# Kernel tuning notes

Hardware: AMD Instinct MI355X
Metric: run time of the kernel (lower is better)

## Reference

```python
import jax, jax.numpy as jnp
import numpy as np

# dims
B, N, L = 8, 128, 512          # batch, n_vars, context_window
PL, ST = 16, 8                  # patch_len, stride
PN = (L - PL) // ST + 1         # patch_num = 63
DM, H, DFF, NL = 128, 16, 256, 2
DK = DM // H
DG, MP, BETA = 8, 3, 0.05       # d_gcn, mp_layers, propbeta
TW = 96                         # target_window


def setup_inputs() -> dict:
    key = jax.random.key(0)
    ks = iter(jax.random.split(key, 64))
    def nrm(shape, s=0.02):
        return jax.random.normal(next(ks), shape, jnp.float32) * s
    inp = {
        "x": jax.random.normal(next(ks), (B, N, L), jnp.float32),
        "adj_logits": jax.random.normal(next(ks), (B, L, N, N), jnp.float32),
        # DGCN params
        "dgcn_start_w": nrm((1, DG)), "dgcn_start_b": jnp.zeros((DG,), jnp.float32),
        "dgcn_mlp_w": nrm(((MP + 1) * DG, 1)), "dgcn_mlp_b": jnp.zeros((1,), jnp.float32),
        # patch embedding + positional
        "W_P": nrm((PL, DM)), "b_P": jnp.zeros((DM,), jnp.float32), "W_pos": nrm((PN, DM)),
        # encoder layers (stacked over NL)
        "Wq": nrm((NL, DM, DM)), "bq": jnp.zeros((NL, DM), jnp.float32),
        "Wk": nrm((NL, DM, DM)), "bk": jnp.zeros((NL, DM), jnp.float32),
        "Wv": nrm((NL, DM, DM)), "bv": jnp.zeros((NL, DM), jnp.float32),
        "Wo": nrm((NL, DM, DM)), "bo": jnp.zeros((NL, DM), jnp.float32),
        "scale": jnp.full((NL,), DK ** -0.5, jnp.float32),
        "bn1_g": jnp.ones((NL, DM), jnp.float32), "bn1_b": jnp.zeros((NL, DM), jnp.float32),
        "ff_w1": nrm((NL, DM, DFF)), "ff_b1": jnp.zeros((NL, DFF), jnp.float32),
        "ff_w2": nrm((NL, DFF, DM)), "ff_b2": jnp.zeros((NL, DM), jnp.float32),
        "bn2_g": jnp.ones((NL, DM), jnp.float32), "bn2_b": jnp.zeros((NL, DM), jnp.float32),
        # head
        "head_w": nrm((DM * PN, TW)), "head_b": jnp.zeros((TW,), jnp.float32),
    }
    return inp


def _bn(x, g, b):
    # BatchNorm1d in training mode over (batch, seq) per feature channel
    mu = x.mean(axis=(0, 1))
    var = x.var(axis=(0, 1))
    return (x - mu) * jax.lax.rsqrt(var + 1e-5) * g + b


def reference(x, adj_logits, dgcn_start_w, dgcn_start_b, dgcn_mlp_w, dgcn_mlp_b,
              W_P, b_P, W_pos, Wq, bq, Wk, bk, Wv, bv, Wo, bo, scale,
              bn1_g, bn1_b, ff_w1, ff_b1, ff_w2, ff_b2, bn2_g, bn2_b,
              head_w, head_b):
    # ---- DGCN: multi-hop diffusion over variables, per time step ----
    x4 = x[..., None]                                   # [b,n,s,1]
    A = jax.nn.softmax(adj_logits, axis=2)              # [b,s,n,m], normalized over source n
    a = jnp.transpose(A, (0, 2, 3, 1))                  # [b,n,m,s]
    h = x4 @ dgcn_start_w + dgcn_start_b                # [b,n,s,d_gcn]
    outs = [h]
    for _ in range(MP):
        h = BETA * x4 + (1.0 - BETA) * jnp.einsum('bnsc,bnms->bmsc', h, a)
        outs.append(h)
    y = (jnp.concatenate(outs, axis=-1) @ dgcn_mlp_w + dgcn_mlp_b)[..., 0]  # [b,n,s]
    # ---- patching ----
    win = jnp.arange(PN)[:, None] * ST + jnp.arange(PL)[None, :]
    z = y[:, :, win]                                    # [b,n,pn,pl]
    # ---- TSTiEncoder (channel independent) ----
    src = (z @ W_P + b_P).reshape(B * N, PN, DM) + W_pos
    prev = None
    for l in range(NL):
        q = (src @ Wq[l] + bq[l]).reshape(-1, PN, H, DK).transpose(0, 2, 1, 3)
        k = (src @ Wk[l] + bk[l]).reshape(-1, PN, H, DK).transpose(0, 2, 1, 3)
        v = (src @ Wv[l] + bv[l]).reshape(-1, PN, H, DK).transpose(0, 2, 1, 3)
        scores = jnp.einsum('bhqd,bhkd->bhqk', q, k) * scale[l]
        if prev is not None:
            scores = scores + prev                      # residual attention
        w = jax.nn.softmax(scores, axis=-1)
        o = jnp.einsum('bhqk,bhkd->bhqd', w, v).transpose(0, 2, 1, 3).reshape(-1, PN, DM)
        src = _bn(src + (o @ Wo[l] + bo[l]), bn1_g[l], bn1_b[l])
        ff = jax.nn.gelu(src @ ff_w1[l] + ff_b1[l], approximate=False) @ ff_w2[l] + ff_b2[l]
        src = _bn(src + ff, bn2_g[l], bn2_b[l])
        prev = scores
    # ---- Flatten_Head ----
    enc = src.reshape(B, N, PN, DM).transpose(0, 1, 3, 2).reshape(B, N, DM * PN)
    return enc @ head_w + head_b                        # [b, n_vars, target_window]
```

## Files before the change

kernel.cpp:

```cpp
#include <hip/hip_runtime.h>
#include <hip/hip_bf16.h>
#include <math.h>

#define RM 64512

typedef short short8 __attribute__((ext_vector_type(8)));
typedef float f32x4 __attribute__((ext_vector_type(4)));
typedef unsigned short ushort4v __attribute__((ext_vector_type(4)));
typedef unsigned short ushort8v __attribute__((ext_vector_type(8)));

__device__ __forceinline__ float gelu_f(float v) {
    return 0.5f * v * (1.0f + erff(v * 0.70710678118654752f));
}
__device__ __forceinline__ float b2f(unsigned short u) {
    unsigned int x = ((unsigned int)u) << 16;
    return __builtin_bit_cast(float, x);
}
__device__ __forceinline__ unsigned short f2b(float f) {
    __hip_bfloat16 h = __float2bfloat16(f);
    return __builtin_bit_cast(unsigned short, h);
}

__global__ __launch_bounds__(256) void dgcn_kernel(
    const float* __restrict__ x, const float* __restrict__ adj,
    const float* __restrict__ sw, const float* __restrict__ sb,
    const float* __restrict__ mw, const float* __restrict__ mb,
    float* __restrict__ y,
    const float* __restrict__ Wq, const float* __restrict__ Wk, const float* __restrict__ Wv,
    const float* __restrict__ Wo, const float* __restrict__ fw1, const float* __restrict__ fw2,
    const float* __restrict__ bq, const float* __restrict__ bk, const float* __restrict__ bv,
    unsigned short* __restrict__ WB, float* __restrict__ bcat)
{
    if (blockIdx.x >= 4096) {
        const int wb = blockIdx.x - 4096;
        const int id = wb / 64, bx = wb % 64;
        const int l = id / 6, mat = id % 6;
        const float* src; int K, N; size_t off = (size_t)l * 131072;
        switch (mat) {
            case 0: src = Wq  + l*16384; K = 128; N = 128; off += 0;      break;
            case 1: src = Wk  + l*16384; K = 128; N = 128; off += 16384;  break;
            case 2: src = Wv  + l*16384; K = 128; N = 128; off += 32768;  break;
            case 3: src = Wo  + l*16384; K = 128; N = 128; off += 49152;  break;
            case 4: src = fw1 + l*32768; K = 128; N = 256; off += 65536;  break;
            default:src = fw2 + l*32768; K = 256; N = 128; off += 98304;  break;
        }
        const int total = K * N;
        const int ksh = (K == 256) ? 8 : 7;
        for (int idx = bx*256 + threadIdx.x; idx < total; idx += 64*256) {
            int n = idx >> ksh, k = idx & (K - 1);
            WB[off + idx] = f2b(src[(size_t)k*N + n]);
        }
        if (id == 0 && bx == 0) {
            for (int idx = threadIdx.x; idx < 768; idx += 256) {
                int ll = idx / 384, j = idx % 384;
                float vv;
                if (j < 128)      vv = bq[ll*128 + j];
                else if (j < 256) vv = bk[ll*128 + j - 128];
                else              vv = bv[ll*128 + j - 256];
                bcat[idx] = vv;
            }
        }
        return;
    }
    __shared__ __align__(16) unsigned short ET[128*128];
    __shared__ __align__(16) unsigned short hT[16*128];
    __shared__ float red[256];
    __shared__ float iv[128];
    __shared__ float xc[128];
    __shared__ float yac[128];
    const int bid = blockIdx.x;
    const int b = bid >> 9, s = bid & 511;
    const int t = threadIdx.x;
    const int lane = t & 63, wid = t >> 6;
    const float* ap = adj + (size_t)bid * 16384;

    if (t < 128) xc[t] = x[((size_t)b*128 + t)*512 + s];

    {
        const int m = t & 127, ng = t >> 7;
        float sm = 0.f;
        for (int p = 0; p < 16; ++p) {
            const int n0 = p*8 + ng*4;
            float e0 = __expf(ap[(size_t)(n0+0)*128 + m]);
            float e1 = __expf(ap[(size_t)(n0+1)*128 + m]);
            float e2 = __expf(ap[(size_t)(n0+2)*128 + m]);
            float e3 = __expf(ap[(size_t)(n0+3)*128 + m]);
            sm += e0 + e1 + e2 + e3;
            ushort4v u4; u4[0]=f2b(e0); u4[1]=f2b(e1); u4[2]=f2b(e2); u4[3]=f2b(e3);
            *(ushort4v*)((char*)ET + m*256 + (((n0>>3) ^ (m & 15))*16) + (n0 & 7)*2) = u4;
        }
        red[ng*128 + m] = sm;
        *(ushort4v*)&hT[8*128 + t*4] = (ushort4v){0,0,0,0};
    }
    __syncthreads();
    if (t < 128) iv[t] = 1.f / (red[t] + red[128 + t]);
    if (t < 128) {
        const int m = t;
        const float xm = xc[m];
        float yp = 0.f;
        #pragma unroll
        for (int c = 0; c < 8; ++c) {
            float h = xm*sw[c] + sb[c];
            yp += h*mw[c];
            *(unsigned short*)((char*)hT + c*256 + ((((m>>3) ^ c))*16) + (m & 7)*2) = f2b(h);
        }
        yac[m] = yp;
    }
    __syncthreads();

    const int rl = lane & 15, kh = lane >> 4;
    short8 af[2][4];
    float xr[2][4], ivr[2][4];
    #pragma unroll
    for (int ti = 0; ti < 2; ++ti) {
        const int mrow = (wid*2 + ti)*16 + rl;
        #pragma unroll
        for (int ks = 0; ks < 4; ++ks) {
            const int ch = (ks*4 + kh) ^ (mrow & 15);
            af[ti][ks] = *(const short8*)((const char*)ET + mrow*256 + ch*16);
        }
        #pragma unroll
        for (int r = 0; r < 4; ++r) {
            const int m = (wid*2 + ti)*16 + kh*4 + r;
            xr[ti][r]  = 0.05f * xc[m];
            ivr[ti][r] = 0.95f * iv[m];
        }
    }
    float yl[2][4] = {};
    #pragma unroll
    for (int step = 1; step <= 3; ++step) {
        short8 bfr[4];
        #pragma unroll
        for (int ks = 0; ks < 4; ++ks) {
            const int ch = (ks*4 + kh) ^ rl;
            bfr[ks] = *(const short8*)((const char*)hT + rl*256 + ch*16);
        }
        f32x4 acc[2] = {};
        #pragma unroll
        for (int ti = 0; ti < 2; ++ti)
            #pragma unroll
            for (int ks = 0; ks < 4; ++ks)
                acc[ti] = __builtin_amdgcn_mfma_f32_16x16x32_bf16(af[ti][ks], bfr[ks], acc[ti], 0, 0, 0);
        __syncthreads();
        const float mwc = (rl < 8) ? mw[step*8 + rl] : 0.f;
        #pragma unroll
        for (int ti = 0; ti < 2; ++ti) {
            const int m0 = (wid*2 + ti)*16 + kh*4;
            ushort4v hw4;
            float hnew[4];
            #pragma unroll
            for (int r = 0; r < 4; ++r) {
                float v = xr[ti][r] + ivr[ti][r]*acc[ti][r];
                hnew[r] = v;
                hw4[r] = f2b(v);
            }
            *(ushort4v*)((char*)hT + rl*256 + (((m0>>3) ^ rl)*16) + (m0 & 7)*2) = hw4;
            #pragma unroll
            for (int r = 0; r < 4; ++r) {
                float vv = hnew[r]*mwc;
                vv += __shfl_xor(vv, 1);
                vv += __shfl_xor(vv, 2);
                vv += __shfl_xor(vv, 4);
                vv += __shfl_xor(vv, 8);
                yl[ti][r] += vv;
            }
        }
        __syncthreads();
    }
    if (rl == 0) {
        #pragma unroll
        for (int ti = 0; ti < 2; ++ti)
            #pragma unroll
            for (int r = 0; r < 4; ++r)
                yac[(wid*2 + ti)*16 + kh*4 + r] += yl[ti][r];
    }
    __syncthreads();
    if (t < 128) y[((size_t)b*128 + t)*512 + s] = yac[t] + mb[0];
}

__global__ __launch_bounds__(256) void patch_kernel(
    const float* __restrict__ y, const float* __restrict__ Wp, const float* __restrict__ bp,
    const float* __restrict__ Wpos, unsigned short* __restrict__ srcb)
{
    __shared__ float ys[512];
    __shared__ float wps[16*128];
    const int bn = blockIdx.x;
    const int t = threadIdx.x;
    ys[t]       = y[(size_t)bn*512 + t];
    ys[t + 256] = y[(size_t)bn*512 + t + 256];
    #pragma unroll
    for (int r = 0; r < 8; ++r) wps[t + r*256] = Wp[t + r*256];
    __syncthreads();
    for (int cu = t; cu < 1008; cu += 256) {
        int p = cu >> 4, d0 = (cu & 15) * 8;
        float o[8];
        #pragma unroll
        for (int j = 0; j < 8; ++j) o[j] = bp[d0+j] + Wpos[p*128 + d0 + j];
        #pragma unroll
        for (int tt = 0; tt < 16; ++tt) {
            float a = ys[p*8 + tt];
            #pragma unroll
            for (int j = 0; j < 8; ++j) o[j] += a * wps[tt*128 + d0 + j];
        }
        size_t row = (size_t)bn*63 + p;
        ushort8v u;
        #pragma unroll
        for (int j = 0; j < 8; ++j) u[j] = f2b(o[j]);
        *(ushort8v*)&srcb[row*128 + d0] = u;
    }
}

template<int ACT, int OM, int RESMODE, bool STATS, bool AHM, int NB, int KK>
__global__ __launch_bounds__(256) void mgemm(
    const unsigned short* __restrict__ A, const unsigned short* __restrict__ WB,
    const float* __restrict__ bias, const unsigned short* __restrict__ Rsd,
    const float* __restrict__ snR,
    unsigned short* __restrict__ Cb,
    float* __restrict__ part)
{
    constexpr int NTOT = NB * 128;
    constexpr int kch = KK >> 3;
    constexpr int KT = KK >> 7;
    __shared__ __align__(16) unsigned short AsL[64*128];
    __shared__ __align__(16) unsigned short BsL[128*128];
    __shared__ float sred[4][16][8], qred[4][16][8];
    const int t = threadIdx.x;
    const int lane = t & 63, wid = t >> 6;
    const int wr = wid >> 1, wc = wid & 1;
    const int m0 = blockIdx.x * 64;
    const int kh = lane >> 4, rl = lane & 15;
    const int rq = lane >> 4;
    float sj[8] = {}, qj[8] = {};

    for (int ib = 0; ib < NB; ++ib) {
        f32x4 acc[2][4] = {};
        for (int kt = 0; kt < KT; ++kt) {
            if (ib == 0 || KT > 1) {
                #pragma unroll
                for (int i = 0; i < 4; ++i) {
                    int cid = i*256 + t;
                    const unsigned short* ga;
                    if constexpr (AHM) {
                        int hd2 = cid >> 6, row = cid & 63;
                        ga = A + ((size_t)hd2*RM + (m0+row))*8;
                    } else {
                        int row = cid >> 4, c = cid & 15;
                        int c_g = c ^ (row & 7);
                        ga = A + ((size_t)(m0+row)*kch + kt*16 + c_g)*8;
                    }
                    __builtin_amdgcn_global_load_lds((const unsigned int*)ga,
                        (unsigned int*)&AsL[(i*256 + wid*64)*8], 16, 0, 0);
                }
            }
            #pragma unroll
            for (int i = 0; i < 8; ++i) {
                int cid = i*256 + t;
                int nr = cid >> 4, c = cid & 15;
                const unsigned short* gb = WB + (size_t)ib*128*KK
                    + ((size_t)nr*kch + kt*16 + (c ^ (nr & 7)))*8;
                __builtin_amdgcn_global_load_lds((const unsigned int*)gb,
                    (unsigned int*)&BsL[(i*256 + wid*64)*8], 16, 0, 0);
            }
            __syncthreads();
            #pragma unroll
            for (int ks = 0; ks < 4; ++ks) {
                const int cA = ks*4 + kh;
                short8 af[2], bfr[4];
                #pragma unroll
                for (int i = 0; i < 2; ++i) {
                    int row = wr*32 + i*16 + rl;
                    if constexpr (AHM) af[i] = *(const short8*)&AsL[(cA*64 + row)*8];
                    else               af[i] = *(const short8*)&AsL[row*128 + ((cA ^ (row & 7))*8)];
                }
                #pragma unroll
                for (int j = 0; j < 4; ++j) {
                    int cn = wc*64 + j*16 + rl;
                    bfr[j] = *(const short8*)&BsL[cn*128 + ((cA ^ (cn & 7))*8)];
                }
                #pragma unroll
                for (int i = 0; i < 2; ++i)
                    #pragma unroll
                    for (int j = 0; j < 4; ++j)
                        acc[i][j] = __builtin_amdgcn_mfma_f32_16x16x32_bf16(af[i], bfr[j], acc[i][j], 0, 0, 0);
            }
            __syncthreads();
        }
        #pragma unroll
        for (int j = 0; j < 4; ++j) {
            const int col_l = wc*64 + j*16 + rl;
            const float bs = bias[ib*128 + col_l];
            const int chunk = col_l >> 3, bo2 = (col_l & 7) << 1;
            #pragma unroll
            for (int i = 0; i < 2; ++i) {
                #pragma unroll
                for (int r = 0; r < 4; ++r) {
                    const int row_l = wr*32 + i*16 + rq*4 + r;
                    float v = acc[i][j][r] + bs;
                    if constexpr (ACT == 1) v = gelu_f(v);
                    *(unsigned short*)((char*)BsL + row_l*256 + ((chunk ^ (row_l & 15))<<4) + bo2) = f2b(v);
                }
            }
        }
        __syncthreads();
        if constexpr (OM == 1) {
            #pragma unroll
            for (int it = 0; it < 4; ++it) {
                int cid = it*256 + t;
                int row_l = cid & 63, hd_l = cid >> 6;
                ushort8v u = *(const ushort8v*)((const char*)BsL + row_l*256 + ((hd_l ^ (row_l & 15))<<4));
                *(ushort8v*)&Cb[(((size_t)(ib*16 + hd_l))*RM + m0 + row_l)*8] = u;
            }
        } else {
            #pragma unroll
            for (int it = 0; it < 4; ++it) {
                const int row_l = it*16 + (t >> 4), c = t & 15;
                ushort8v u = *(const ushort8v*)((const char*)BsL + row_l*256 + ((c ^ (row_l & 15))<<4));
                const size_t gbase = (size_t)(m0 + row_l)*NTOT + ib*128 + c*8;
                ushort8v rs = {};
                if constexpr (RESMODE != 0) rs = *(const ushort8v*)&Rsd[gbase];
                ushort8v o8;
                #pragma unroll
                for (int jj = 0; jj < 8; ++jj) {
                    float v = b2f(u[jj]);
                    if constexpr (RESMODE == 1) v += b2f(rs[jj]);
                    if constexpr (RESMODE == 2) v += b2f(rs[jj])*snR[c*8+jj] + snR[128 + c*8 + jj];
                    if constexpr (STATS) { sj[jj] += v; qj[jj] += v*v; }
                    o8[jj] = f2b(v);
                }
                *(ushort8v*)&Cb[gbase] = o8;
            }
        }
        __syncthreads();
    }
    if constexpr (STATS) {
        #pragma unroll
        for (int jj = 0; jj < 8; ++jj) {
            sj[jj] += __shfl_xor(sj[jj], 16); qj[jj] += __shfl_xor(qj[jj], 16);
            sj[jj] += __shfl_xor(sj[jj], 32); qj[jj] += __shfl_xor(qj[jj], 32);
        }
        if ((lane >> 4) == 0) {
            #pragma unroll
            for (int jj = 0; jj < 8; ++jj) {
                sred[wid][lane][jj] = sj[jj];
                qred[wid][lane][jj] = qj[jj];
            }
        }
        __syncthreads();
        if (t < 128) {
            const int c2 = t >> 3, jj = t & 7;
            float s = sred[0][c2][jj] + sred[1][c2][jj] + sred[2][c2][jj] + sred[3][c2][jj];
            float q = qred[0][c2][jj] + qred[1][c2][jj] + qred[2][c2][jj] + qred[3][c2][jj];
            part[(size_t)blockIdx.x*256 + t]       = s;
            part[(size_t)blockIdx.x*256 + 128 + t] = q;
        }
    }
}

__global__ __launch_bounds__(256) void bnred(const float* __restrict__ part,
    const float* __restrict__ g, const float* __restrict__ b, float* __restrict__ sn)
{
    const int c = blockIdx.x, t = threadIdx.x;
    float s = 0.f, q = 0.f;
    for (int bid = t; bid < 1008; bid += 256) {
        s += part[(size_t)bid*256 + c];
        q += part[(size_t)bid*256 + 128 + c];
    }
    __shared__ float ls[256], lq[256];
    ls[t] = s; lq[t] = q;
    __syncthreads();
    for (int o = 128; o > 0; o >>= 1) {
        if (t < o) { ls[t] += ls[t+o]; lq[t] += lq[t+o]; }
        __syncthreads();
    }
    if (t == 0) {
        const float invM = 1.f / (float)RM;
        float mean = ls[0] * invM;
        float var  = fmaxf(lq[0]*invM - mean*mean, 0.f);
        float sc = g[c] * rsqrtf(var + 1e-5f);
        sn[c]       = sc;
        sn[128 + c] = b[c] - mean*sc;
    }
}

__global__ __launch_bounds__(256) void wfold(const unsigned short* __restrict__ WBs,
    const float* __restrict__ sn, const float* __restrict__ bsrc,
    unsigned short* __restrict__ WBd, float* __restrict__ bdst)
{
    const int t = threadIdx.x, wv = t >> 6, lane = t & 63;
    const int n = blockIdx.x*4 + wv;
    float w1 = b2f(WBs[(size_t)n*128 + lane]);
    float w2 = b2f(WBs[(size_t)n*128 + 64 + lane]);
    WBd[(size_t)n*128 + lane]      = f2b(sn[lane]*w1);
    WBd[(size_t)n*128 + 64 + lane] = f2b(sn[64+lane]*w2);
    float bacc = sn[128+lane]*w1 + sn[192+lane]*w2;
    #pragma unroll
    for (int msk = 1; msk < 64; msk <<= 1) bacc += __shfl_xor(bacc, msk);
    if (lane == 0) bdst[n] = bsrc[n] + bacc;
}

template<int L>
__global__ __launch_bounds__(256) void attn_kernel(
    const unsigned short* __restrict__ qkv, const unsigned short* __restrict__ qkvP,
    const float* __restrict__ scale, unsigned short* __restrict__ ob)
{
    __shared__ float ks[4][504], vs[4][504], k0s[4][504];
    const int bn = blockIdx.x;
    const int t = threadIdx.x, wid = t >> 6, lane = t & 63;
    const int hd = blockIdx.y*4 + wid;
    const size_t rbase = (size_t)hd*RM + (size_t)bn*63;
    float qr[8] = {}, q0r[8] = {};
    if (lane < 63) {
        ushort8v ku = *(const ushort8v*)&qkv[((size_t)16*RM*8) + (rbase + lane)*8];
        ushort8v vu = *(const ushort8v*)&qkv[((size_t)32*RM*8) + (rbase + lane)*8];
        #pragma unroll
        for (int d = 0; d < 8; ++d) { ks[wid][lane*8+d] = b2f(ku[d]); vs[wid][lane*8+d] = b2f(vu[d]); }
        ushort8v qu = *(const ushort8v*)&qkv[(rbase + lane)*8];
        #pragma unroll
        for (int d = 0; d < 8; ++d) qr[d] = b2f(qu[d]);
        if constexpr (L > 0) {
            ushort8v k0u = *(const ushort8v*)&qkvP[((size_t)16*RM*8) + (rbase + lane)*8];
            #pragma unroll
            for (int d = 0; d < 8; ++d) k0s[wid][lane*8+d] = b2f(k0u[d]);
            ushort8v q0u = *(const ushort8v*)&qkvP[(rbase + lane)*8];
            #pragma unroll
            for (int d = 0; d < 8; ++d) q0r[d] = b2f(q0u[d]);
        }
    }
    __syncthreads();
    if (lane >= 63) return;
    const float scl  = scale[L];
    const float scl0 = (L > 0) ? scale[0] : 0.f;
    float sum = 0.f;
    float oa[8] = {};
    for (int j = 0; j < 63; ++j) {
        float s = 0.f;
        #pragma unroll
        for (int d = 0; d < 8; ++d) s += qr[d]*ks[wid][j*8+d];
        s *= scl;
        if constexpr (L > 0) {
            float s0 = 0.f;
            #pragma unroll
            for (int d = 0; d < 8; ++d) s0 += q0r[d]*k0s[wid][j*8+d];
            s += scl0 * s0;
        }
        float p = __expf(s);
        sum += p;
        #pragma unroll
        for (int d = 0; d < 8; ++d) oa[d] += p*vs[wid][j*8+d];
    }
    float inv = 1.f / sum;
    ushort8v u;
    #pragma unroll
    for (int d = 0; d < 8; ++d) u[d] = f2b(oa[d]*inv);
    *(ushort8v*)&ob[((size_t)hd*RM + (size_t)bn*63 + lane)*8] = u;
}

__global__ __launch_bounds__(256) void hprep(
    const float* __restrict__ hw, const float* __restrict__ hb,
    const float* __restrict__ sn,
    unsigned short* __restrict__ hwTf, float* __restrict__ hbf)
{
    const int t = threadIdx.x;
    if (blockIdx.x < 63) {
        const int p = blockIdx.x;
        for (int idx = t; idx < 16384; idx += 256) {
            int n = idx >> 7, d = idx & 127;
            unsigned short w = 0;
            if (n < 96) w = f2b(sn[d] * hw[(size_t)(d*63 + p)*96 + n]);
            hwTf[((size_t)p*128 + n)*128 + d] = w;
        }
    } else {
        const int n = blockIdx.x - 63;
        float acc = 0.f;
        for (int k = t; k < 8064; k += 256) {
            int d = (int)(((unsigned)k * 33289u) >> 21);
            acc += sn[128 + d] * hw[(size_t)k*96 + n];
        }
        __shared__ float ls[256];
        ls[t] = acc;
        __syncthreads();
        for (int o = 128; o > 0; o >>= 1) { if (t < o) ls[t] += ls[t+o]; __syncthreads(); }
        if (t == 0) hbf[n] = hb[n] + ls[0];
    }
}

__global__ __launch_bounds__(256) void mhead(
    const unsigned short* __restrict__ A, const unsigned short* __restrict__ BW,
    float* __restrict__ part)
{
    __shared__ __align__(16) unsigned short AsL[128*128];
    __shared__ __align__(16) unsigned short BsL[128*128];
    const int t = threadIdx.x;
    const int lane = t & 63, wid = t >> 6;
    const int wr = wid >> 1, wc = wid & 1;
    const int m0 = blockIdx.x * 128;
    const int p  = blockIdx.y;
    #pragma unroll
    for (int i = 0; i < 8; ++i) {
        int cid = i*256 + t;
        int row = cid >> 4, c = cid & 15;
        const unsigned short* ga = A + ((size_t)(m0+row)*63 + p)*128 + ((c ^ (row & 7))*8);
        __builtin_amdgcn_global_load_lds((const unsigned int*)ga,
            (unsigned int*)&AsL[(i*256 + wid*64)*8], 16, 0, 0);
    }
    #pragma unroll
    for (int i = 0; i < 8; ++i) {
        int cid = i*256 + t;
        int nr = cid >> 4, c = cid & 15;
        const unsigned short* gb = BW + ((size_t)p*128 + nr)*128 + ((c ^ (nr & 7))*8);
        __builtin_amdgcn_global_load_lds((const unsigned int*)gb,
            (unsigned int*)&BsL[(i*256 + wid*64)*8], 16, 0, 0);
    }
    __syncthreads();
    const int kh = lane >> 4, rl = lane & 15;
    f32x4 acc[4][3] = {};
    #pragma unroll
    for (int kq = 0; kq < 4; ++kq) {
        const int cA = kq*4 + kh;
        short8 af[4], bfr[3];
        #pragma unroll
        for (int i = 0; i < 4; ++i) {
            int row = wr*64 + i*16 + rl;
            af[i] = *(const short8*)&AsL[row*128 + ((cA ^ (row & 7))*8)];
        }
        #pragma unroll
        for (int j = 0; j < 3; ++j) {
            int cn = wc*48 + j*16 + rl;
            bfr[j] = *(const short8*)&BsL[cn*128 + ((cA ^ (cn & 7))*8)];
        }
        #pragma unroll
        for (int i = 0; i < 4; ++i)
            #pragma unroll
            for (int j = 0; j < 3; ++j)
                acc[i][j] = __builtin_amdgcn_mfma_f32_16x16x32_bf16(af[i], bfr[j], acc[i][j], 0, 0, 0);
    }
    const int rl2 = lane & 15, rq = lane >> 4;
    #pragma unroll
    for (int j = 0; j < 3; ++j) {
        const int col = wc*48 + j*16 + rl2;
        #pragma unroll
        for (int i = 0; i < 4; ++i) {
            const int rbase = m0 + wr*64 + i*16 + rq*4;
            #pragma unroll
            for (int r = 0; r < 4; ++r)
                part[((size_t)p*1024 + rbase + r)*96 + col] = acc[i][j][r];
        }
    }
}

__global__ __launch_bounds__(256) void head_reduce(const float* __restrict__ part,
    const float* __restrict__ hbf, float* __restrict__ out)
{
    int idx = blockIdx.x*256 + threadIdx.x;
    float s = hbf[idx % 96];
    #pragma unroll
    for (int blk = 0; blk < 63; ++blk) s += part[(size_t)blk*98304 + idx];
    out[idx] = s;
}

extern "C" void kernel_launch(void* const* d_in, const int* in_sizes, int n_in,
                              void* d_out, int out_size, void* d_ws, size_t ws_size,
                              hipStream_t stream) {
    const float* x    = (const float*)d_in[0];
    const float* adj  = (const float*)d_in[1];
    const float* sw   = (const float*)d_in[2];
    const float* sb   = (const float*)d_in[3];
    const float* mw   = (const float*)d_in[4];
    const float* mb   = (const float*)d_in[5];
    const float* Wp   = (const float*)d_in[6];
    const float* bp   = (const float*)d_in[7];
    const float* Wpos = (const float*)d_in[8];
    const float* Wq   = (const float*)d_in[9];
    const float* bq   = (const float*)d_in[10];
    const float* Wk   = (const float*)d_in[11];
    const float* bk   = (const float*)d_in[12];
    const float* Wv   = (const float*)d_in[13];
    const float* bv   = (const float*)d_in[14];
    const float* Wo   = (const float*)d_in[15];
    const float* bo   = (const float*)d_in[16];
    const float* scale= (const float*)d_in[17];
    const float* bn1g = (const float*)d_in[18];
    const float* bn1b = (const float*)d_in[19];
    const float* fw1  = (const float*)d_in[20];
    const float* fb1  = (const float*)d_in[21];
    const float* fw2  = (const float*)d_in[22];
    const float* fb2  = (const float*)d_in[23];
    const float* bn2g = (const float*)d_in[24];
    const float* bn2b = (const float*)d_in[25];
    const float* hw   = (const float*)d_in[26];
    const float* hb   = (const float*)d_in[27];
    float* out = (float*)d_out;

    float* y     = (float*)d_ws;
    float* part  = y     + 524288;
    float* snorm = part  + 258048;
    float* bcat  = snorm + 1024;
    float* bfold = bcat  + 768;
    float* hbf   = bfold + 1024;
    float* hpart = hbf   + 128;
    unsigned short* srcb = (unsigned short*)(hpart + 6193152);
    unsigned short* t1b  = srcb + 8257536;
    unsigned short* t2b  = t1b  + 8257536;
    unsigned short* g    = t2b  + 8257536;
    unsigned short* o_bf = g    + 16515072;
    unsigned short* qkv0 = o_bf + 8257536;
    unsigned short* qkv1 = qkv0 + 24772608;
    unsigned short* WB   = qkv1 + 24772608;
    unsigned short* WF   = WB   + 262144;
    unsigned short* hwTf = WF   + 131072;

    dgcn_kernel<<<4864, 256, 0, stream>>>(x, adj, sw, sb, mw, mb, y,
        Wq, Wk, Wv, Wo, fw1, fw2, bq, bk, bv, WB, bcat);
    patch_kernel<<<1024, 256, 0, stream>>>(y, Wp, bp, Wpos, srcb);

    mgemm<0,1,0,false,false,3,128><<<1008, 256, 0, stream>>>(srcb, WB, bcat, nullptr, nullptr, qkv0, nullptr);
    attn_kernel<0><<<dim3(1024,4), 256, 0, stream>>>(qkv0, qkv0, scale, o_bf);
    mgemm<0,2,1,true,true,1,128><<<1008, 256, 0, stream>>>(o_bf, WB + 49152, bo, srcb, nullptr, t1b, part);
    bnred<<<128, 256, 0, stream>>>(part, bn1g, bn1b, snorm);
    wfold<<<64, 256, 0, stream>>>(WB + 65536, snorm, fb1, WF, bfold);
    mgemm<1,2,0,false,false,2,128><<<1008, 256, 0, stream>>>(t1b, WF, bfold, nullptr, nullptr, g, nullptr);
    mgemm<0,2,2,true,false,1,256><<<1008, 256, 0, stream>>>(g, WB + 98304, fb2, t1b, snorm, t2b, part);
    bnred<<<128, 256, 0, stream>>>(part, bn2g, bn2b, snorm + 256);
    wfold<<<96, 256, 0, stream>>>(WB + 131072, snorm + 256, bcat + 384, WF + 65536, bfold + 512);

    mgemm<0,1,0,false,false,3,128><<<1008, 256, 0, stream>>>(t2b, WF + 65536, bfold + 512, nullptr, nullptr, qkv1, nullptr);
    attn_kernel<1><<<dim3(1024,4), 256, 0, stream>>>(qkv1, qkv0, scale, o_bf);
    mgemm<0,2,2,true,true,1,128><<<1008, 256, 0, stream>>>(o_bf, WB + 131072 + 49152, bo + 128, t2b, snorm + 256, t1b, part);
    bnred<<<128, 256, 0, stream>>>(part, bn1g + 128, bn1b + 128, snorm + 512);
    wfold<<<64, 256, 0, stream>>>(WB + 131072 + 65536, snorm + 512, fb1 + 256, WF + 32768, bfold + 256);
    mgemm<1,2,0,false,false,2,128><<<1008, 256, 0, stream>>>(t1b, WF + 32768, bfold + 256, nullptr, nullptr, g, nullptr);
    mgemm<0,2,2,true,false,1,256><<<1008, 256, 0, stream>>>(g, WB + 131072 + 98304, fb2 + 128, t1b, snorm + 512, t2b, part);
    bnred<<<128, 256, 0, stream>>>(part, bn2g + 128, bn2b + 128, snorm + 768);

    hprep<<<159, 256, 0, stream>>>(hw, hb, snorm + 768, hwTf, hbf);
    mhead<<<dim3(8,63), 256, 0, stream>>>(t2b, hwTf, hpart);
    head_reduce<<<384, 256, 0, stream>>>(hpart, hbf, out);
}
```

Measured before the change: 393.2 us.

## Fuse FFN up-projection, GELU and down-projection into one kernel

Replaces the two feed-forward GEMM launches per layer with a single kernel. It computes the 256-wide GELU hidden tile for 64 rows, keeps it in shared memory, and multiplies it by W2 in place. The residual add and the BatchNorm partial-sum epilogue are kept in the same kernel. This removes the global write and re-read of the large hidden activation tensor g and one launch per layer. The cost is 80KB of shared memory per block, which lowers occupancy, and W1 and W2 loads are serialised rather than pipelined.

```diff
diff --git a/kernel.cpp b/kernel.cpp
--- a/kernel.cpp
+++ b/kernel.cpp
@@ -353,6 +353,183 @@
             part[(size_t)blockIdx.x*256 + t]       = s;
             part[(size_t)blockIdx.x*256 + 128 + t] = q;
         }
+    }
+}
+
+__global__ __launch_bounds__(256) void ffused(
+    const unsigned short* __restrict__ A, const unsigned short* __restrict__ W1,
+    const float* __restrict__ b1, const unsigned short* __restrict__ W2,
+    const float* __restrict__ b2, const unsigned short* __restrict__ Rsd,
+    const float* __restrict__ snR,
+    unsigned short* __restrict__ Cb, float* __restrict__ part)
+{
+    __shared__ __align__(16) char smem[81920];
+    unsigned short* AsL = (unsigned short*)smem;
+    unsigned short* BsL = (unsigned short*)(smem + 16384);
+    unsigned short* G   = (unsigned short*)(smem + 49152);
+    float* sred = (float*)(smem + 49152);
+    float* qred = sred + 512;
+    const int t = threadIdx.x;
+    const int lane = t & 63, wid = t >> 6;
+    const int wr = wid >> 1, wc = wid & 1;
+    const int m0 = blockIdx.x * 64;
+    const int kh = lane >> 4, rl = lane & 15;
+    const int rq = lane >> 4;
+
+    #pragma unroll
+    for (int i = 0; i < 4; ++i) {
+        int cid = i*256 + t;
+        int row = cid >> 4, c = cid & 15;
+        const unsigned short* ga = A + ((size_t)(m0+row)*16 + (c ^ (row & 7)))*8;
+        __builtin_amdgcn_global_load_lds((const unsigned int*)ga,
+            (unsigned int*)&AsL[(i*256 + wid*64)*8], 16, 0, 0);
+    }
+    #pragma unroll
+    for (int i = 0; i < 8; ++i) {
+        int cid = i*256 + t;
+        int nr = cid >> 4, c = cid & 15;
+        const unsigned short* gb = W1 + ((size_t)nr*16 + (c ^ (nr & 7)))*8;
+        __builtin_amdgcn_global_load_lds((const unsigned int*)gb,
+            (unsigned int*)&BsL[(i*256 + wid*64)*8], 16, 0, 0);
+    }
+    __syncthreads();
+    for (int ib = 0; ib < 2; ++ib) {
+        f32x4 acc[2][4] = {};
+        #pragma unroll
+        for (int ks = 0; ks < 4; ++ks) {
+            const int cA = ks*4 + kh;
+            short8 af[2], bfr[4];
+            #pragma unroll
+            for (int i = 0; i < 2; ++i) {
+                int row = wr*32 + i*16 + rl;
+                af[i] = *(const short8*)&AsL[row*128 + ((cA ^ (row & 7))*8)];
+            }
+            #pragma unroll
+            for (int j = 0; j < 4; ++j) {
+                int cn = wc*64 + j*16 + rl;
+                bfr[j] = *(const short8*)&BsL[cn*128 + ((cA ^ (cn & 7))*8)];
+            }
+            #pragma unroll
+            for (int i = 0; i < 2; ++i)
+                #pragma unroll
+                for (int j = 0; j < 4; ++j)
+                    acc[i][j] = __builtin_amdgcn_mfma_f32_16x16x32_bf16(af[i], bfr[j], acc[i][j], 0, 0, 0);
+        }
+        __syncthreads();
+        if (ib == 0) {
+            #pragma unroll
+            for (int i = 0; i < 8; ++i) {
+                int cid = i*256 + t;
+                int nr = cid >> 4, c = cid & 15;
+                const unsigned short* gb = W1 + ((size_t)(128+nr)*16 + (c ^ (nr & 7)))*8;
+                __builtin_amdgcn_global_load_lds((const unsigned int*)gb,
+                    (unsigned int*)&BsL[(i*256 + wid*64)*8], 16, 0, 0);
+            }
+        }
+        #pragma unroll
+        for (int j = 0; j < 4; ++j) {
+            const int col_l = wc*64 + j*16 + rl;
+            const int colg = ib*128 + col_l;
+            const float bs = b1[colg];
+            const int cg = colg >> 3, bo2 = (colg & 7) << 1;
+            #pragma unroll
+            for (int i = 0; i < 2; ++i) {
+                #pragma unroll
+                for (int r = 0; r < 4; ++r) {
+                    const int row_l = wr*32 + i*16 + rq*4 + r;
+                    float v = gelu_f(acc[i][j][r] + bs);
+                    *(unsigned short*)((char*)G + row_l*512 + (((cg ^ (row_l & 15)))<<4) + bo2) = f2b(v);
+                }
+            }
+        }
+        __syncthreads();
+    }
+    f32x4 acc2[2][4] = {};
+    for (int kt = 0; kt < 2; ++kt) {
+        #pragma unroll
+        for (int i = 0; i < 8; ++i) {
+            int cid = i*256 + t;
+            int nr = cid >> 4, c = cid & 15;
+            const unsigned short* gb = W2 + ((size_t)nr*32 + kt*16 + (c ^ (nr & 7)))*8;
+            __builtin_amdgcn_global_load_lds((const unsigned int*)gb,
+                (unsigned int*)&BsL[(i*256 + wid*64)*8], 16, 0, 0);
+        }
+        __syncthreads();
+        #pragma unroll
+        for (int ks = 0; ks < 4; ++ks) {
+            const int cA = ks*4 + kh;
+            short8 af[2], bfr[4];
+            #pragma unroll
+            for (int i = 0; i < 2; ++i) {
+                int row = wr*32 + i*16 + rl;
+                af[i] = *(const short8*)((const char*)G + row*512 + ((((kt*16 + cA) ^ (row & 15)))<<4));
+            }
+            #pragma unroll
+            for (int j = 0; j < 4; ++j) {
+                int cn = wc*64 + j*16 + rl;
+                bfr[j] = *(const short8*)&BsL[cn*128 + ((cA ^ (cn & 7))*8)];
+            }
+            #pragma unroll
+            for (int i = 0; i < 2; ++i)
+                #pragma unroll
+                for (int j = 0; j < 4; ++j)
+                    acc2[i][j] = __builtin_amdgcn_mfma_f32_16x16x32_bf16(af[i], bfr[j], acc2[i][j], 0, 0, 0);
+        }
+        __syncthreads();
+    }
+    #pragma unroll
+    for (int j = 0; j < 4; ++j) {
+        const int col_l = wc*64 + j*16 + rl;
+        const float bs = b2[col_l];
+        const int chunk = col_l >> 3, bo2 = (col_l & 7) << 1;
+        #pragma unroll
+        for (int i = 0; i < 2; ++i) {
+            #pragma unroll
+            for (int r = 0; r < 4; ++r) {
+                const int row_l = wr*32 + i*16 + rq*4 + r;
+                *(unsigned short*)((char*)AsL + row_l*256 + ((chunk ^ (row_l & 15))<<4) + bo2)
+                    = f2b(acc2[i][j][r] + bs);
+            }
+        }
+    }
+    __syncthreads();
+    float sj[8] = {}, qj[8] = {};
+    #pragma unroll
+    for (int it = 0; it < 4; ++it) {
+        const int row_l = it*16 + (t >> 4), c = t & 15;
+        ushort8v u = *(const ushort8v*)((const char*)AsL + row_l*256 + ((c ^ (row_l & 15))<<4));
+        const size_t gbase = (size_t)(m0 + row_l)*128 + c*8;
+        ushort8v rs = *(const ushort8v*)&Rsd[gbase];
+        ushort8v o8;
+        #pragma unroll
+        for (int jj = 0; jj < 8; ++jj) {
+            float v = b2f(u[jj]) + b2f(rs[jj])*snR[c*8+jj] + snR[128 + c*8 + jj];
+            sj[jj] += v; qj[jj] += v*v;
+            o8[jj] = f2b(v);
+        }
+        *(ushort8v*)&Cb[gbase] = o8;
+    }
+    #pragma unroll
+    for (int jj = 0; jj < 8; ++jj) {
+        sj[jj] += __shfl_xor(sj[jj], 16); qj[jj] += __shfl_xor(qj[jj], 16);
+        sj[jj] += __shfl_xor(sj[jj], 32); qj[jj] += __shfl_xor(qj[jj], 32);
+    }
+    if ((lane >> 4) == 0) {
+        #pragma unroll
+        for (int jj = 0; jj < 8; ++jj) {
+            sred[wid*128 + lane*8 + jj] = sj[jj];
+            qred[wid*128 + lane*8 + jj] = qj[jj];
+        }
+    }
+    __syncthreads();
+    if (t < 128) {
+        const int c2 = t >> 3, jj = t & 7;
+        float s = sred[0*128 + c2*8 + jj] + sred[1*128 + c2*8 + jj]
+                + sred[2*128 + c2*8 + jj] + sred[3*128 + c2*8 + jj];
+        float q = qred[0*128 + c2*8 + jj] + qred[1*128 + c2*8 + jj]
+                + qred[2*128 + c2*8 + jj] + qred[3*128 + c2*8 + jj];
+        part[(size_t)blockIdx.x*256 + t]       = s;
+        part[(size_t)blockIdx.x*256 + 128 + t] = q;
     }
 }
 
@@ -618,8 +795,7 @@
     mgemm<0,2,1,true,true,1,128><<<1008, 256, 0, stream>>>(o_bf, WB + 49152, bo, srcb, nullptr, t1b, part);
     bnred<<<128, 256, 0, stream>>>(part, bn1g, bn1b, snorm);
     wfold<<<64, 256, 0, stream>>>(WB + 65536, snorm, fb1, WF, bfold);
-    mgemm<1,2,0,false,false,2,128><<<1008, 256, 0, stream>>>(t1b, WF, bfold, nullptr, nullptr, g, nullptr);
-    mgemm<0,2,2,true,false,1,256><<<1008, 256, 0, stream>>>(g, WB + 98304, fb2, t1b, snorm, t2b, part);
+    ffused<<<1008, 256, 0, stream>>>(t1b, WF, bfold, WB + 98304, fb2, t1b, snorm, t2b, part);
     bnred<<<128, 256, 0, stream>>>(part, bn2g, bn2b, snorm + 256);
     wfold<<<96, 256, 0, stream>>>(WB + 131072, snorm + 256, bcat + 384, WF + 65536, bfold + 512);
 
@@ -628,8 +804,7 @@
     mgemm<0,2,2,true,true,1,128><<<1008, 256, 0, stream>>>(o_bf, WB + 131072 + 49152, bo + 128, t2b, snorm + 256, t1b, part);
     bnred<<<128, 256, 0, stream>>>(part, bn1g + 128, bn1b + 128, snorm + 512);
     wfold<<<64, 256, 0, stream>>>(WB + 131072 + 65536, snorm + 512, fb1 + 256, WF + 32768, bfold + 256);
-    mgemm<1,2,0,false,false,2,128><<<1008, 256, 0, stream>>>(t1b, WF + 32768, bfold + 256, nullptr, nullptr, g, nullptr);
-    mgemm<0,2,2,true,false,1,256><<<1008, 256, 0, stream>>>(g, WB + 131072 + 98304, fb2 + 128, t1b, snorm + 512, t2b, part);
+    ffused<<<1008, 256, 0, stream>>>(t1b, WF + 32768, bfold + 256, WB + 131072 + 98304, fb2 + 128, t1b, snorm + 512, t2b, part);
     bnred<<<128, 256, 0, stream>>>(part, bn2g + 128, bn2b + 128, snorm + 768);
 
     hprep<<<159, 256, 0, stream>>>(hw, hb, snorm + 768, hwTf, hbf);
```

New measurement: 373.1 us, median of 2. 1.05x faster.
